# Performance work log

Measured on AMD Instinct MI355X. Metric: run time of the kernel, lower is better.

## Reference

```python
import jax, jax.numpy as jnp
import numpy as np

B, N, F_IN, H = 16, 1024, 64, 256
NEG = -9e15
ALPHA = 0.2  # LeakyReLU slope


def _leaky(x):
    return jnp.where(x >= 0, x, ALPHA * x)


def setup_inputs() -> dict:
    key = jax.random.key(0)
    ks = jax.random.split(key, 12)
    s = lambda k, shape, fan: jax.random.normal(k, shape, jnp.float32) / np.sqrt(fan)
    node_features = jax.random.normal(ks[0], (B, N, F_IN), jnp.float32)
    adj_matrix = jax.random.randint(ks[1], (B, N, N), 0, 2).astype(jnp.float32)
    return {
        "node_features": node_features,
        "adj_matrix": adj_matrix,
        "emb_W": s(ks[2], (F_IN, H), F_IN),
        "emb_b": jnp.zeros((H,), jnp.float32),
        "W0": s(ks[3], (H, H), H),
        "a1_0": s(ks[4], (H,), H),
        "a2_0": s(ks[5], (H,), H),
        "W1": s(ks[6], (H, H), H),
        "a1_1": s(ks[7], (H,), H),
        "a2_1": s(ks[8], (H,), H),
        "gp_W1": s(ks[9], (H, H), H),
        "gp_b1": jnp.zeros((H,), jnp.float32),
        "gp_W2": s(ks[10], (H, H), H),
        "gp_b2": jnp.zeros((H,), jnp.float32),
    }


def _gat_layer(x, mask, W, a1, a2):
    # x: [B,N,H]; mask: [B,N,N] bool. Equivalent to original concat trick:
    # a([h_i || h_j]) = h_i @ a1 + h_j @ a2 with a.weight split in halves.
    h = jnp.einsum('bnf,fo->bno', x, W)              # [B,N,H]
    s1 = jnp.einsum('bnh,h->bn', h, a1)              # [B,N]
    s2 = jnp.einsum('bnh,h->bn', h, a2)              # [B,N]
    e = _leaky(s1[:, :, None] + s2[:, None, :])      # [B,N,N]
    att = jax.nn.softmax(jnp.where(mask, e, NEG), axis=2)
    # dropout p=0.2 is identity in eval mode
    return jnp.einsum('bij,bjh->bih', att, h)        # [B,N,H]


def reference(node_features, adj_matrix, emb_W, emb_b,
              W0, a1_0, a2_0, W1, a1_1, a2_1,
              gp_W1, gp_b1, gp_W2, gp_b2):
    mask = adj_matrix > 0
    x = jnp.einsum('bnf,fh->bnh', node_features, emb_W) + emb_b
    x = jax.nn.relu(_gat_layer(x, mask, W0, a1_0, a2_0))
    x = jax.nn.relu(_gat_layer(x, mask, W1, a1_1, a2_1))
    g = jnp.mean(x, axis=1) + jnp.max(x, axis=1)     # [B,H]
    g = jax.nn.relu(g @ gp_W1 + gp_b1) @ gp_W2 + gp_b2
    return x, g
```

## Files before the change

kernel.cpp:

```cpp
#include <hip/hip_runtime.h>
#include <hip/hip_bf16.h>

#define B 16
#define N 1024
#define F_IN 64
#define H 256
#define ALPHA 0.2f
#define LOG2E 1.44269504f

typedef __attribute__((ext_vector_type(8))) _Float16 half8;
typedef __attribute__((ext_vector_type(4))) _Float16 half4;
typedef __attribute__((ext_vector_type(4))) float floatx4;

#if __has_builtin(__builtin_amdgcn_exp2f)
#define EXP2F(x) __builtin_amdgcn_exp2f(x)
#else
#define EXP2F(x) exp2f(x)
#endif

__device__ __forceinline__ floatx4 mfma_f16(half8 a, half8 b, floatx4 c) {
    return __builtin_amdgcn_mfma_f32_16x16x32_f16(a, b, c, 0, 0, 0);
}

__global__ __launch_bounds__(256) void k_front(const float* __restrict__ adj,
                                               const float* __restrict__ nf,
                                               const float* __restrict__ embW,
                                               const float* __restrict__ embB,
                                               const float* __restrict__ W0, const float* __restrict__ W1,
                                               const float* __restrict__ a10, const float* __restrict__ a20,
                                               const float* __restrict__ a11, const float* __restrict__ a21,
                                               unsigned* __restrict__ mask32,
                                               _Float16* __restrict__ xf,
                                               _Float16* __restrict__ wBf,
                                               float* __restrict__ wa1, float* __restrict__ wa2) {
    __shared__ float lds[256 * 17];
    const int blk = blockIdx.x;
    const int t = threadIdx.x;
    const int lane = t & 63;

    if (blk < 1024) {
        const int wv = blk * 4 + (t >> 6);
#pragma unroll 2
        for (int task = wv; task < B * N * 4; task += 4096) {
            const float4 v = *(const float4*)(adj + (size_t)task * 256 + lane * 4);
            unsigned long long b0 = __ballot(v.x > 0.f);
            unsigned long long b1 = __ballot(v.y > 0.f);
            unsigned long long b2 = __ballot(v.z > 0.f);
            unsigned long long b3 = __ballot(v.w > 0.f);
            if (lane < 8) {
                unsigned w0 = (unsigned)((b0 >> (8 * lane)) & 0xff)
                            | ((unsigned)((b1 >> (8 * lane)) & 0xff) << 8)
                            | ((unsigned)((b2 >> (8 * lane)) & 0xff) << 16)
                            | ((unsigned)((b3 >> (8 * lane)) & 0xff) << 24);
                const int jg = task & 3, row = task >> 2;
                mask32[(size_t)row * 32 + jg * 8 + lane] = w0;
            }
        }
        return;
    }
    if (blk < 1536) {
        const int row0 = (blk - 1024) * 32;
        float* nfs = lds;
        for (int idx = t; idx < 32 * F_IN; idx += 256) {
            int r = idx >> 6, f = idx & 63;
            nfs[f * 32 + r] = nf[(size_t)(row0 + r) * F_IN + f];
        }
        __syncthreads();
        const int c = t;
        float acc[32];
        const float bv = embB[c];
#pragma unroll
        for (int r = 0; r < 32; r++) acc[r] = bv;
#pragma unroll 8
        for (int f = 0; f < F_IN; f++) {
            const float w = embW[f * H + c];
            const float* nrow = nfs + f * 32;
#pragma unroll
            for (int q = 0; q < 8; q++) {
                float4 n4 = *(const float4*)(nrow + q * 4);
                acc[q * 4 + 0] += n4.x * w;
                acc[q * 4 + 1] += n4.y * w;
                acc[q * 4 + 2] += n4.z * w;
                acc[q * 4 + 3] += n4.w * w;
            }
        }
#pragma unroll
        for (int r = 0; r < 32; r++)
            xf[(size_t)(row0 + r) * H + c] = (_Float16)acc[r];
        return;
    }
    const int pb = blk - 1536;
    if (pb >= 32) {
        const int l = pb - 32;
        const float* W = l ? W1 : W0;
        const float* a1 = l ? a11 : a10;
        const float* a2 = l ? a21 : a20;
        float* a1s = lds;
        float* a2s = lds + 256;
        a1s[t] = a1[t]; a2s[t] = a2[t];
        __syncthreads();
        float v1 = 0.f, v2 = 0.f;
        for (int c = 0; c < H; c += 4) {
            float4 w = *(const float4*)&W[t * H + c];
            v1 += w.x * a1s[c] + w.y * a1s[c + 1] + w.z * a1s[c + 2] + w.w * a1s[c + 3];
            v2 += w.x * a2s[c] + w.y * a2s[c + 1] + w.z * a2s[c + 2] + w.w * a2s[c + 3];
        }
        wa1[l * H + t] = v1;
        wa2[l * H + t] = v2;
        return;
    }
    const int l = pb >> 4, ct = pb & 15;
    const float* W = l ? W1 : W0;
#pragma unroll
    for (int rep = 0; rep < 16; rep++) {
        int idx = rep * 256 + t;
        int k = idx >> 4, cl = idx & 15;
        lds[k * 17 + cl] = W[k * H + ct * 16 + cl];
    }
    __syncthreads();
    const int w = t >> 6;
    const int l15 = lane & 15, quad = lane >> 4;
#pragma unroll
    for (int e = 0; e < 2; e++) {
        const int ks = w * 2 + e;
        half8 bf;
#pragma unroll
        for (int jj = 0; jj < 8; jj++)
            bf[jj] = (_Float16)lds[(ks * 32 + quad * 8 + jj) * 17 + l15];
        *(half8*)(wBf + (size_t)(((l * 16 + ct) * 8 + ks) * 64 + lane) * 8) = bf;
    }
}

#define XS(it, ks) ((((it) * 8 + (ks))) * 520)
__global__ __launch_bounds__(256, 4) void k_gemm(const _Float16* __restrict__ xf,
                                                 const _Float16* __restrict__ wBf,
                                                 const float* __restrict__ wa1, const float* __restrict__ wa2,
                                                 _Float16* __restrict__ hB,
                                                 float* __restrict__ s1, float* __restrict__ s2) {
    __shared__ __align__(16) _Float16 sm[8320];
    const int lin = blockIdx.x;
    const int rc = lin >> 1, chalf = lin & 1;
    const int row0 = rc * 32;
    const int t = threadIdx.x;
    const int lane = t & 63, w = t >> 6;
    const int l15 = lane & 15, quad = lane >> 4;

#pragma unroll
    for (int pass = 0; pass < 4; pass++) {
        int idx = pass * 256 + t;
        int row_l = idx >> 5, k8 = idx & 31;
        half8 v = *(const half8*)(xf + (size_t)(row0 + row_l) * H + k8 * 8);
        int it = row_l >> 4, lf = row_l & 15, ks = k8 >> 2, qd = k8 & 3;
        *(half8*)(sm + XS(it, ks) + (qd * 16 + lf) * 8) = v;
    }
    __syncthreads();

    const int ct0 = chalf * 8 + 2 * w;
    const _Float16* pB0 = wBf + (size_t)((ct0 * 8) * 64 + lane) * 8;
    const _Float16* pB1 = wBf + (size_t)(((ct0 + 1) * 8) * 64 + lane) * 8;

    floatx4 acc[2][2];
    floatx4 z = {0.f, 0.f, 0.f, 0.f};
    acc[0][0] = z; acc[0][1] = z; acc[1][0] = z; acc[1][1] = z;
    float sp1a = 0.f, sp2a = 0.f, sp1b = 0.f, sp2b = 0.f;

    half8 B0 = *(const half8*)(pB0);
    half8 B1 = *(const half8*)(pB1);

#pragma unroll
    for (int ks = 0; ks < 8; ks++) {
        half8 nB0 = B0, nB1 = B1;
        if (ks < 7) {
            const int o = (ks + 1) * 512;
            nB0 = *(const half8*)(pB0 + o);
            nB1 = *(const half8*)(pB1 + o);
        }
        half8 A0 = *(const half8*)(sm + XS(0, ks) + lane * 8);
        half8 A1 = *(const half8*)(sm + XS(1, ks) + lane * 8);
        acc[0][0] = mfma_f16(A0, B0, acc[0][0]);
        acc[0][1] = mfma_f16(A0, B1, acc[0][1]);
        acc[1][0] = mfma_f16(A1, B0, acc[1][0]);
        acc[1][1] = mfma_f16(A1, B1, acc[1][1]);
        if (chalf == 0 && w == 0) {
            float4 w1a = *(const float4*)(wa1 + ks * 32 + quad * 8);
            float4 w1b = *(const float4*)(wa1 + ks * 32 + quad * 8 + 4);
            float4 w2a = *(const float4*)(wa2 + ks * 32 + quad * 8);
            float4 w2b = *(const float4*)(wa2 + ks * 32 + quad * 8 + 4);
            float wv1[8] = {w1a.x, w1a.y, w1a.z, w1a.w, w1b.x, w1b.y, w1b.z, w1b.w};
            float wv2[8] = {w2a.x, w2a.y, w2a.z, w2a.w, w2b.x, w2b.y, w2b.z, w2b.w};
#pragma unroll
            for (int j = 0; j < 8; j++) {
                float xa = (float)A0[j];
                float xb = (float)A1[j];
                sp1a += xa * wv1[j]; sp2a += xa * wv2[j];
                sp1b += xb * wv1[j]; sp2b += xb * wv2[j];
            }
        }
        B0 = nB0; B1 = nB1;
    }

    __syncthreads();
    _Float16* trc = sm;
#pragma unroll
    for (int rg = 0; rg < 2; rg++) {
#pragma unroll
        for (int n2 = 0; n2 < 2; n2++) {
            const int c_l = (2 * w + n2) * 16 + l15;
            half4 hv;
            hv[0] = (_Float16)acc[rg][n2][0];
            hv[1] = (_Float16)acc[rg][n2][1];
            hv[2] = (_Float16)acc[rg][n2][2];
            hv[3] = (_Float16)acc[rg][n2][3];
            *(half4*)(trc + c_l * 40 + rg * 16 + quad * 4) = hv;
        }
    }
    __syncthreads();
    {
        const int ct_l = t >> 5, sub = t & 31;
        const int bb = row0 >> 10, jt = (row0 >> 5) & 31;
        _Float16* dst = hB + (size_t)(((bb * 16 + chalf * 8 + ct_l) * 32 + jt) * 64) * 8;
#pragma unroll
        for (int rep = 0; rep < 2; rep++) {
            int lo = sub + rep * 32;
            int qd = lo >> 4, lf = lo & 15;
            half8 hv = *(const half8*)(trc + (ct_l * 16 + lf) * 40 + qd * 8);
            *(half8*)(dst + lo * 8) = hv;
        }
    }
    if (chalf == 0 && w == 0) {
        sp1a += __shfl_xor(sp1a, 16); sp1a += __shfl_xor(sp1a, 32);
        sp2a += __shfl_xor(sp2a, 16); sp2a += __shfl_xor(sp2a, 32);
        sp1b += __shfl_xor(sp1b, 16); sp1b += __shfl_xor(sp1b, 32);
        sp2b += __shfl_xor(sp2b, 16); sp2b += __shfl_xor(sp2b, 32);
        if (quad == 0) {
            s1[row0 + l15] = sp1a; s2[row0 + l15] = sp2a;
            s1[row0 + 16 + l15] = sp1b; s2[row0 + 16 + l15] = sp2b;
        }
    }
}

template <int LAST>
__global__ __launch_bounds__(256, 2) void k_gat(const _Float16* __restrict__ hB,
                                                const float* __restrict__ s1g,
                                                const float* __restrict__ s2g,
                                                const unsigned* __restrict__ mask32,
                                                float* __restrict__ outf,
                                                _Float16* __restrict__ oxf,
                                                float* __restrict__ psum, float* __restrict__ pmax) {
    __shared__ float s2s[N];
    __shared__ unsigned msk[64][33];
    __shared__ float wmax[4];
    __shared__ float red1[4][128];
    __shared__ float red2[4][128];
    const int lin = blockIdx.x;
    const int xcd = lin & 7, sl = lin >> 3;
    const int b = xcd * 2 + (sl & 1);
    const int chunk = (sl >> 1) & 15;
    const int chalf = sl >> 5;
    const int i0 = chunk * 64;
    const int t = threadIdx.x;
    const int lane = t & 63, w = t >> 6;
    const int l15 = lane & 15, quad = lane >> 4;
    const int ct0 = chalf * 8;

    float tm = -INFINITY;
    for (int idx = t; idx < N; idx += 256) {
        float v = s2g[b * N + idx] * LOG2E;
        s2s[idx] = v;
        tm = fmaxf(tm, v);
    }
#pragma unroll
    for (int off = 1; off <= 32; off <<= 1) tm = fmaxf(tm, __shfl_xor(tm, off));
    if (lane == 0) wmax[w] = tm;
#pragma unroll
    for (int pass = 0; pass < 8; pass++) {
        int idx = pass * 256 + t;
        int r = idx >> 5, wd = idx & 31;
        msk[r][wd] = mask32[(size_t)(b * N + i0 + r) * 32 + wd];
    }
    __syncthreads();
    const float s2maxL = fmaxf(fmaxf(wmax[0], wmax[1]), fmaxf(wmax[2], wmax[3]));

    const float s1L = s1g[b * N + i0 + w * 16 + l15] * LOG2E;
    const float tmx = s1L + s2maxL;
    const float mL = fmaxf(tmx, ALPHA * tmx);
    const float a1c = s1L - mL;
    const float a2c = fmaf(ALPHA, s1L, -mL);

    const _Float16* pb[8];
#pragma unroll
    for (int k = 0; k < 8; k++)
        pb[k] = hB + (size_t)((b * 16 + ct0 + k) * 32 * 64) * 8 + lane * 8;

    floatx4 acc[8];
    floatx4 z = {0.f, 0.f, 0.f, 0.f};
#pragma unroll
    for (int k = 0; k < 8; k++) acc[k] = z;
    floatx4 accl = z;

    half8 ones;
#pragma unroll
    for (int jj = 0; jj < 8; jj++) ones[jj] = (_Float16)1.0f;

    const float* svp = s2s + quad * 8;
    const unsigned* mr = &msk[w * 16 + l15][0];

    half8 bufA[8], bufB[8];
#pragma unroll
    for (int k = 0; k < 8; k++) bufA[k] = *(const half8*)(pb[k]);

#define GAT_STEP(JT, BUF)                                                      \
    do {                                                                       \
        float4 sa = *(const float4*)(svp + (JT) * 32);                         \
        float4 sb = *(const float4*)(svp + (JT) * 32 + 4);                     \
        float sv[8] = {sa.x, sa.y, sa.z, sa.w, sb.x, sb.y, sb.z, sb.w};        \
        unsigned mq = mr[JT] >> (quad * 2);                                    \
        union { _Float16 h[8]; half8 v; } pk;                                  \
        _Pragma("unroll")                                                      \
        for (int jj = 0; jj < 8; jj++) {                                       \
            const int bp = (jj & 3) * 8 + (jj >> 2);                           \
            float u = a1c + sv[jj];                                            \
            float v2 = fmaf(ALPHA, sv[jj], a2c);                               \
            float e = fmaxf(u, v2);                                            \
            e = ((mq >> bp) & 1u) ? e : -126.f;                                \
            pk.h[jj] = (_Float16)EXP2F(e);                                     \
        }                                                                      \
        accl = mfma_f16(pk.v, ones, accl);                                     \
        _Pragma("unroll")                                                      \
        for (int k = 0; k < 8; k++) acc[k] = mfma_f16(pk.v, BUF[k], acc[k]);   \
    } while (0)

    for (int jt = 0; jt < 32; jt += 2) {
        {
            const int o = (jt + 1) * 512;
#pragma unroll
            for (int k = 0; k < 8; k++) bufB[k] = *(const half8*)(pb[k] + o);
        }
        GAT_STEP(jt, bufA);
        if (jt + 2 < 32) {
            const int o = (jt + 2) * 512;
#pragma unroll
            for (int k = 0; k < 8; k++) bufA[k] = *(const half8*)(pb[k] + o);
        }
        GAT_STEP(jt + 1, bufB);
    }
#undef GAT_STEP

    float inv[4];
#pragma unroll
    for (int r = 0; r < 4; r++) inv[r] = 1.f / accl[r];

    const size_t rbase = (size_t)b * N + i0 + w * 16 + quad * 4;
#pragma unroll
    for (int k = 0; k < 8; k++) {
        const int c = (ct0 + k) * 16 + l15;
        float cs = 0.f, cm = -INFINITY;
#pragma unroll
        for (int r = 0; r < 4; r++) {
            float v = fmaxf(acc[k][r] * inv[r], 0.f);
            if (LAST) {
                outf[(rbase + r) * H + c] = v;
                cs += v; cm = fmaxf(cm, v);
            } else {
                oxf[(rbase + r) * H + c] = (_Float16)v;
            }
        }
        if (LAST) {
            cs += __shfl_xor(cs, 16); cs += __shfl_xor(cs, 32);
            cm = fmaxf(cm, __shfl_xor(cm, 16)); cm = fmaxf(cm, __shfl_xor(cm, 32));
            if (quad == 0) { red1[w][k * 16 + l15] = cs; red2[w][k * 16 + l15] = cm; }
        }
    }
    if (LAST) {
        __syncthreads();
        if (t < 128) {
            float s = red1[0][t] + red1[1][t] + red1[2][t] + red1[3][t];
            float m = fmaxf(fmaxf(red2[0][t], red2[1][t]), fmaxf(red2[2][t], red2[3][t]));
            psum[(b * 16 + chunk) * H + chalf * 128 + t] = s;
            pmax[(b * 16 + chunk) * H + chalf * 128 + t] = m;
        }
    }
}

__global__ __launch_bounds__(256) void k_pool2(const float* __restrict__ psum,
                                               const float* __restrict__ pmax,
                                               const float* __restrict__ W1, const float* __restrict__ b1,
                                               const float* __restrict__ W2, const float* __restrict__ b2,
                                               float* __restrict__ gout) {
    __shared__ float g_s[H];
    __shared__ float t_s[H];
    const int b = blockIdx.x;
    const int c = threadIdx.x;
    float s = 0.f, m = -INFINITY;
#pragma unroll
    for (int ch = 0; ch < 16; ch++) {
        s += psum[(b * 16 + ch) * H + c];
        m = fmaxf(m, pmax[(b * 16 + ch) * H + c]);
    }
    g_s[c] = s * (1.f / N) + m;
    __syncthreads();
    float a = b1[c];
#pragma unroll 16
    for (int k = 0; k < H; k++) a += g_s[k] * W1[k * H + c];
    t_s[c] = fmaxf(a, 0.f);
    __syncthreads();
    float o = b2[c];
#pragma unroll 16
    for (int k = 0; k < H; k++) o += t_s[k] * W2[k * H + c];
    gout[b * H + c] = o;
}

extern "C" void kernel_launch(void* const* d_in, const int* in_sizes, int n_in,
                              void* d_out, int out_size, void* d_ws, size_t ws_size,
                              hipStream_t stream) {
    const float* nf    = (const float*)d_in[0];
    const float* adj   = (const float*)d_in[1];
    const float* emb_W = (const float*)d_in[2];
    const float* emb_b = (const float*)d_in[3];
    const float* W0    = (const float*)d_in[4];
    const float* a1_0  = (const float*)d_in[5];
    const float* a2_0  = (const float*)d_in[6];
    const float* W1    = (const float*)d_in[7];
    const float* a1_1  = (const float*)d_in[8];
    const float* a2_1  = (const float*)d_in[9];
    const float* gpW1  = (const float*)d_in[10];
    const float* gpb1  = (const float*)d_in[11];
    const float* gpW2  = (const float*)d_in[12];
    const float* gpb2  = (const float*)d_in[13];

    float* xout = (float*)d_out;
    float* gout = xout + B * N * H;

    char* w = (char*)d_ws;
    _Float16* xf     = (_Float16*)(w);
    _Float16* hB     = (_Float16*)(w + 8388608);
    unsigned* mask32 = (unsigned*)(w + 16777216);
    float* s1        = (float*)(w + 18874368);
    float* s2        = (float*)(w + 18939904);
    _Float16* wBf    = (_Float16*)(w + 19005440);
    float* wa1       = (float*)(w + 19267584);
    float* wa2       = (float*)(w + 19269632);
    float* psum      = (float*)(w + 19271680);
    float* pmax      = (float*)(w + 19533824);

    k_front<<<1570, 256, 0, stream>>>(adj, nf, emb_W, emb_b, W0, W1,
                                      a1_0, a2_0, a1_1, a2_1,
                                      mask32, xf, wBf, wa1, wa2);

    k_gemm<<<1024, 256, 0, stream>>>(xf, wBf, wa1, wa2, hB, s1, s2);
    k_gat<0><<<512, 256, 0, stream>>>(hB, s1, s2, mask32, nullptr, xf,
                                      nullptr, nullptr);

    k_gemm<<<1024, 256, 0, stream>>>(xf, wBf + 65536, wa1 + H, wa2 + H, hB, s1, s2);
    k_gat<1><<<512, 256, 0, stream>>>(hB, s1, s2, mask32, xout, nullptr,
                                      psum, pmax);

    k_pool2<<<B, 256, 0, stream>>>(psum, pmax, gpW1, gpb1, gpW2, gpb2, gout);
}
```

Baseline: 221.2 us.

## Switch GAT attention to 32x32x16 MFMA with 128-row tiles

The fused attention kernel now uses 32x32x16 f16 MFMA tiles instead of 16x16x32, so each block handles 128 query rows rather than 64 and each wave covers 32 rows. The GEMM epilogue writes the h operand in a new fragment layout that matches the larger MFMA B operand, and the pooling partials shrink to 8 chunks per batch. This is meant to halve the exp/softmax work and B-operand reloads per output and to get more MFMA throughput per instruction. The cost is a grid of only 256 blocks at one block per CU, which may leave CUs idle and hide latency less well, plus more accumulator registers per thread.

```diff
diff --git a/kernel.cpp b/kernel.cpp
--- a/kernel.cpp
+++ b/kernel.cpp
@@ -11,6 +11,7 @@
 typedef __attribute__((ext_vector_type(8))) _Float16 half8;
 typedef __attribute__((ext_vector_type(4))) _Float16 half4;
 typedef __attribute__((ext_vector_type(4))) float floatx4;
+typedef __attribute__((ext_vector_type(16))) float floatx16;
 
 #if __has_builtin(__builtin_amdgcn_exp2f)
 #define EXP2F(x) __builtin_amdgcn_exp2f(x)
@@ -20,6 +21,9 @@
 
 __device__ __forceinline__ floatx4 mfma_f16(half8 a, half8 b, floatx4 c) {
     return __builtin_amdgcn_mfma_f32_16x16x32_f16(a, b, c, 0, 0, 0);
+}
+__device__ __forceinline__ floatx16 mfma32_f16(half8 a, half8 b, floatx16 c) {
+    return __builtin_amdgcn_mfma_f32_32x32x16_f16(a, b, c, 0, 0, 0);
 }
 
 __global__ __launch_bounds__(256) void k_front(const float* __restrict__ adj,
@@ -216,15 +220,17 @@
     }
     __syncthreads();
     {
-        const int ct_l = t >> 5, sub = t & 31;
-        const int bb = row0 >> 10, jt = (row0 >> 5) & 31;
-        _Float16* dst = hB + (size_t)(((bb * 16 + chalf * 8 + ct_l) * 32 + jt) * 64) * 8;
+        const int bb = row0 >> 10, jtb = (row0 >> 5) & 31;
 #pragma unroll
         for (int rep = 0; rep < 2; rep++) {
-            int lo = sub + rep * 32;
-            int qd = lo >> 4, lf = lo & 15;
-            half8 hv = *(const half8*)(trc + (ct_l * 16 + lf) * 40 + qd * 8);
-            *(half8*)(dst + lo * 8) = hv;
+            int slot = rep * 256 + t;
+            int l = slot & 63, frag = slot >> 6;
+            int k4 = frag >> 1, ks = frag & 1;
+            int c_l = k4 * 32 + (l & 31);
+            int roff = ks * 16 + (l >> 5) * 8;
+            half8 hv = *(const half8*)(trc + c_l * 40 + roff);
+            _Float16* dst = hB + ((size_t)((bb * 8 + chalf * 4 + k4) * 32 + jtb) * 2 + ks) * 512 + l * 8;
+            *(half8*)dst = hv;
         }
     }
     if (chalf == 0 && w == 0) {
@@ -240,7 +246,7 @@
 }
 
 template <int LAST>
-__global__ __launch_bounds__(256, 2) void k_gat(const _Float16* __restrict__ hB,
+__global__ __launch_bounds__(256, 1) void k_gat(const _Float16* __restrict__ hB,
                                                 const float* __restrict__ s1g,
                                                 const float* __restrict__ s2g,
                                                 const unsigned* __restrict__ mask32,
@@ -248,20 +254,20 @@
                                                 _Float16* __restrict__ oxf,
                                                 float* __restrict__ psum, float* __restrict__ pmax) {
     __shared__ float s2s[N];
-    __shared__ unsigned msk[64][33];
+    __shared__ unsigned msk[128][33];
     __shared__ float wmax[4];
     __shared__ float red1[4][128];
     __shared__ float red2[4][128];
     const int lin = blockIdx.x;
     const int xcd = lin & 7, sl = lin >> 3;
     const int b = xcd * 2 + (sl & 1);
-    const int chunk = (sl >> 1) & 15;
-    const int chalf = sl >> 5;
-    const int i0 = chunk * 64;
+    const int chunk = (sl >> 1) & 7;
+    const int chalf = sl >> 4;
+    const int i0 = chunk * 128;
     const int t = threadIdx.x;
     const int lane = t & 63, w = t >> 6;
-    const int l15 = lane & 15, quad = lane >> 4;
-    const int ct0 = chalf * 8;
+    const int l31 = lane & 31, hi = lane >> 5;
+    const int hi2 = hi * 2, hi8 = hi * 8;
 
     float tm = -INFINITY;
     for (int idx = t; idx < N; idx += 256) {
@@ -273,7 +279,7 @@
     for (int off = 1; off <= 32; off <<= 1) tm = fmaxf(tm, __shfl_xor(tm, off));
     if (lane == 0) wmax[w] = tm;
 #pragma unroll
-    for (int pass = 0; pass < 8; pass++) {
+    for (int pass = 0; pass < 16; pass++) {
         int idx = pass * 256 + t;
         int r = idx >> 5, wd = idx & 31;
         msk[r][wd] = mask32[(size_t)(b * N + i0 + r) * 32 + wd];
@@ -281,94 +287,121 @@
     __syncthreads();
     const float s2maxL = fmaxf(fmaxf(wmax[0], wmax[1]), fmaxf(wmax[2], wmax[3]));
 
-    const float s1L = s1g[b * N + i0 + w * 16 + l15] * LOG2E;
+    const float s1L = s1g[b * N + i0 + w * 32 + l31] * LOG2E;
     const float tmx = s1L + s2maxL;
     const float mL = fmaxf(tmx, ALPHA * tmx);
     const float a1c = s1L - mL;
     const float a2c = fmaf(ALPHA, s1L, -mL);
 
-    const _Float16* pb[8];
-#pragma unroll
-    for (int k = 0; k < 8; k++)
-        pb[k] = hB + (size_t)((b * 16 + ct0 + k) * 32 * 64) * 8 + lane * 8;
-
-    floatx4 acc[8];
-    floatx4 z = {0.f, 0.f, 0.f, 0.f};
-#pragma unroll
-    for (int k = 0; k < 8; k++) acc[k] = z;
-    floatx4 accl = z;
+    const _Float16* pb[4][2];
+#pragma unroll
+    for (int k4 = 0; k4 < 4; k4++)
+#pragma unroll
+        for (int ks = 0; ks < 2; ks++)
+            pb[k4][ks] = hB + ((size_t)(b * 8 + chalf * 4 + k4) * 64 + ks) * 512 + lane * 8;
+
+    floatx16 acc[4];
+    floatx16 accl;
+#pragma unroll
+    for (int r = 0; r < 16; r++) accl[r] = 0.f;
+#pragma unroll
+    for (int k4 = 0; k4 < 4; k4++) acc[k4] = accl;
 
     half8 ones;
 #pragma unroll
     for (int jj = 0; jj < 8; jj++) ones[jj] = (_Float16)1.0f;
 
-    const float* svp = s2s + quad * 8;
-    const unsigned* mr = &msk[w * 16 + l15][0];
-
-    half8 bufA[8], bufB[8];
-#pragma unroll
-    for (int k = 0; k < 8; k++) bufA[k] = *(const half8*)(pb[k]);
+    const float* svp = s2s + hi8;
+    const unsigned* mr = &msk[w * 32 + l31][0];
+
+    half8 bufA[4][2], bufB[4][2];
+#pragma unroll
+    for (int k4 = 0; k4 < 4; k4++) {
+        bufA[k4][0] = *(const half8*)(pb[k4][0]);
+        bufA[k4][1] = *(const half8*)(pb[k4][1]);
+    }
 
 #define GAT_STEP(JT, BUF)                                                      \
     do {                                                                       \
-        float4 sa = *(const float4*)(svp + (JT) * 32);                         \
-        float4 sb = *(const float4*)(svp + (JT) * 32 + 4);                     \
-        float sv[8] = {sa.x, sa.y, sa.z, sa.w, sb.x, sb.y, sb.z, sb.w};        \
-        unsigned mq = mr[JT] >> (quad * 2);                                    \
-        union { _Float16 h[8]; half8 v; } pk;                                  \
+        const unsigned m = mr[JT];                                             \
+        float4 sa0 = *(const float4*)(svp + (JT) * 32);                        \
+        float4 sb0 = *(const float4*)(svp + (JT) * 32 + 4);                    \
+        float4 sa1 = *(const float4*)(svp + (JT) * 32 + 16);                   \
+        float4 sb1 = *(const float4*)(svp + (JT) * 32 + 20);                   \
+        float sv0[8] = {sa0.x, sa0.y, sa0.z, sa0.w, sb0.x, sb0.y, sb0.z, sb0.w};\
+        float sv1[8] = {sa1.x, sa1.y, sa1.z, sa1.w, sb1.x, sb1.y, sb1.z, sb1.w};\
+        unsigned mq0 = m >> hi2;                                               \
+        unsigned mq1 = m >> (4 + hi2);                                         \
+        union { _Float16 h[8]; half8 v; } pk0, pk1;                            \
         _Pragma("unroll")                                                      \
-        for (int jj = 0; jj < 8; jj++) {                                       \
-            const int bp = (jj & 3) * 8 + (jj >> 2);                           \
-            float u = a1c + sv[jj];                                            \
-            float v2 = fmaf(ALPHA, sv[jj], a2c);                               \
-            float e = fmaxf(u, v2);                                            \
-            e = ((mq >> bp) & 1u) ? e : -126.f;                                \
-            pk.h[jj] = (_Float16)EXP2F(e);                                     \
+        for (int e = 0; e < 8; e++) {                                          \
+            const int bp = (e & 3) * 8 + (e >> 2);                             \
+            float u0 = a1c + sv0[e];                                           \
+            float v0 = fmaf(ALPHA, sv0[e], a2c);                               \
+            float w0 = fmaxf(u0, v0);                                          \
+            w0 = ((mq0 >> bp) & 1u) ? w0 : -126.f;                             \
+            pk0.h[e] = (_Float16)EXP2F(w0);                                    \
+            float u1 = a1c + sv1[e];                                           \
+            float v1 = fmaf(ALPHA, sv1[e], a2c);                               \
+            float w1 = fmaxf(u1, v1);                                          \
+            w1 = ((mq1 >> bp) & 1u) ? w1 : -126.f;                             \
+            pk1.h[e] = (_Float16)EXP2F(w1);                                    \
         }                                                                      \
-        accl = mfma_f16(pk.v, ones, accl);                                     \
+        accl = mfma32_f16(pk0.v, ones, accl);                                  \
         _Pragma("unroll")                                                      \
-        for (int k = 0; k < 8; k++) acc[k] = mfma_f16(pk.v, BUF[k], acc[k]);   \
+        for (int k4 = 0; k4 < 4; k4++) acc[k4] = mfma32_f16(pk0.v, BUF[k4][0], acc[k4]); \
+        accl = mfma32_f16(pk1.v, ones, accl);                                  \
+        _Pragma("unroll")                                                      \
+        for (int k4 = 0; k4 < 4; k4++) acc[k4] = mfma32_f16(pk1.v, BUF[k4][1], acc[k4]); \
     } while (0)
 
     for (int jt = 0; jt < 32; jt += 2) {
         {
-            const int o = (jt + 1) * 512;
-#pragma unroll
-            for (int k = 0; k < 8; k++) bufB[k] = *(const half8*)(pb[k] + o);
+            const int o = (jt + 1) * 1024;
+#pragma unroll
+            for (int k4 = 0; k4 < 4; k4++) {
+                bufB[k4][0] = *(const half8*)(pb[k4][0] + o);
+                bufB[k4][1] = *(const half8*)(pb[k4][1] + o);
+            }
         }
         GAT_STEP(jt, bufA);
         if (jt + 2 < 32) {
-            const int o = (jt + 2) * 512;
-#pragma unroll
-            for (int k = 0; k < 8; k++) bufA[k] = *(const half8*)(pb[k] + o);
+            const int o = (jt + 2) * 1024;
+#pragma unroll
+            for (int k4 = 0; k4 < 4; k4++) {
+                bufA[k4][0] = *(const half8*)(pb[k4][0] + o);
+                bufA[k4][1] = *(const half8*)(pb[k4][1] + o);
+            }
         }
         GAT_STEP(jt + 1, bufB);
     }
 #undef GAT_STEP
 
-    float inv[4];
-#pragma unroll
-    for (int r = 0; r < 4; r++) inv[r] = 1.f / accl[r];
-
-    const size_t rbase = (size_t)b * N + i0 + w * 16 + quad * 4;
-#pragma unroll
-    for (int k = 0; k < 8; k++) {
-        const int c = (ct0 + k) * 16 + l15;
+    float invv[16];
+#pragma unroll
+    for (int r = 0; r < 16; r++) invv[r] = 1.f / accl[r];
+
+    const size_t rowb = (size_t)b * N + i0 + w * 32 + 4 * hi;
+    const int colbase = chalf * 128;
+#pragma unroll
+    for (int k4 = 0; k4 < 4; k4++) {
+        const int c = colbase + k4 * 32 + l31;
         float cs = 0.f, cm = -INFINITY;
 #pragma unroll
-        for (int r = 0; r < 4; r++) {
-            float v = fmaxf(acc[k][r] * inv[r], 0.f);
+        for (int reg = 0; reg < 16; reg++) {
+            const int roff = (reg & 3) + 8 * (reg >> 2);
+            float v = fmaxf(acc[k4][reg] * invv[reg], 0.f);
             if (LAST) {
-                outf[(rbase + r) * H + c] = v;
+                outf[(rowb + roff) * H + c] = v;
                 cs += v; cm = fmaxf(cm, v);
             } else {
-                oxf[(rbase + r) * H + c] = (_Float16)v;
+                oxf[(rowb + roff) * H + c] = (_Float16)v;
             }
         }
         if (LAST) {
-            cs += __shfl_xor(cs, 16); cs += __shfl_xor(cs, 32);
-            cm = fmaxf(cm, __shfl_xor(cm, 16)); cm = fmaxf(cm, __shfl_xor(cm, 32));
-            if (quad == 0) { red1[w][k * 16 + l15] = cs; red2[w][k * 16 + l15] = cm; }
+            cs += __shfl_xor(cs, 32);
+            cm = fmaxf(cm, __shfl_xor(cm, 32));
+            if (hi == 0) { red1[w][k4 * 32 + l31] = cs; red2[w][k4 * 32 + l31] = cm; }
         }
     }
     if (LAST) {
@@ -376,8 +409,8 @@
         if (t < 128) {
             float s = red1[0][t] + red1[1][t] + red1[2][t] + red1[3][t];
             float m = fmaxf(fmaxf(red2[0][t], red2[1][t]), fmaxf(red2[2][t], red2[3][t]));
-            psum[(b * 16 + chunk) * H + chalf * 128 + t] = s;
-            pmax[(b * 16 + chunk) * H + chalf * 128 + t] = m;
+            psum[(b * 8 + chunk) * H + chalf * 128 + t] = s;
+            pmax[(b * 8 + chunk) * H + chalf * 128 + t] = m;
         }
     }
 }
@@ -393,9 +426,9 @@
     const int c = threadIdx.x;
     float s = 0.f, m = -INFINITY;
 #pragma unroll
-    for (int ch = 0; ch < 16; ch++) {
-        s += psum[(b * 16 + ch) * H + c];
-        m = fmaxf(m, pmax[(b * 16 + ch) * H + c]);
+    for (int ch = 0; ch < 8; ch++) {
+        s += psum[(b * 8 + ch) * H + c];
+        m = fmaxf(m, pmax[(b * 8 + ch) * H + c]);
     }
     g_s[c] = s * (1.f / N) + m;
     __syncthreads();
@@ -448,11 +481,11 @@
                                       mask32, xf, wBf, wa1, wa2);
 
     k_gemm<<<1024, 256, 0, stream>>>(xf, wBf, wa1, wa2, hB, s1, s2);
-    k_gat<0><<<512, 256, 0, stream>>>(hB, s1, s2, mask32, nullptr, xf,
+    k_gat<0><<<256, 256, 0, stream>>>(hB, s1, s2, mask32, nullptr, xf,
                                       nullptr, nullptr);
 
     k_gemm<<<1024, 256, 0, stream>>>(xf, wBf + 65536, wa1 + H, wa2 + H, hB, s1, s2);
-    k_gat<1><<<512, 256, 0, stream>>>(hB, s1, s2, mask32, xout, nullptr,
+    k_gat<1><<<256, 256, 0, stream>>>(hB, s1, s2, mask32, xout, nullptr,
                                       psum, pmax);
 
     k_pool2<<<B, 256, 0, stream>>>(psum, pmax, gpW1, gpb1, gpW2, gpb2, gout);
```

Result: no change. 221.3 us (+0.1%).
